# Performance work log

Measured on AMD Instinct MI355X. Metric: run time of the kernel, lower is better.

Reference implementation:

```python
import jax, jax.numpy as jnp
import numpy as np

B, Q, HID = 2, 2048, 2048
HQ, HKV, D = 16, 4, 128
EPS = 1e-6
THETA = 1000000.0


def _rmsnorm(x, w):
    # x: [..., D]
    return x * jax.lax.rsqrt(jnp.mean(x * x, axis=-1, keepdims=True) + EPS) * w


def _rope(x, cos, sin):
    # neox-style: split halves. x: [B,Q,H,D], cos/sin: [B,Q,1,D/2]
    d2 = x.shape[-1] // 2
    x1, x2 = x[..., :d2], x[..., d2:]
    return jnp.concatenate([x1 * cos - x2 * sin, x2 * cos + x1 * sin], axis=-1)


def setup_inputs() -> dict:
    key = jax.random.key(0)
    k1, k2, k3 = jax.random.split(key, 3)
    positions = jnp.broadcast_to(jnp.arange(Q, dtype=jnp.int32), (B, Q))
    hidden_states = jax.random.normal(k1, (B, Q, HID), dtype=jnp.float32)
    k_cache = jnp.zeros((B, HKV, Q, D), dtype=jnp.float32)
    v_cache = jnp.zeros((B, HKV, Q, D), dtype=jnp.float32)
    wqkv = jax.random.normal(k2, (HQ * D + 2 * HKV * D, HID), dtype=jnp.float32) * (HID ** -0.5)
    wo = jax.random.normal(k3, (HID, HQ * D), dtype=jnp.float32) * ((HQ * D) ** -0.5)
    q_norm_w = jnp.ones((D,), dtype=jnp.float32)
    k_norm_w = jnp.ones((D,), dtype=jnp.float32)
    return {"positions": positions, "hidden_states": hidden_states, "k_cache": k_cache,
            "v_cache": v_cache, "wqkv": wqkv, "wo": wo, "q_norm_w": q_norm_w,
            "k_norm_w": k_norm_w, "seq_len": Q}


def reference(positions, hidden_states, k_cache, v_cache, wqkv, wo, q_norm_w, k_norm_w, seq_len):
    bsz, qlen, _ = hidden_states.shape
    q_size, kv_size = HQ * D, HKV * D
    scale = D ** -0.5

    qkv = hidden_states.reshape(bsz * qlen, HID) @ wqkv.T  # [B*Q, q+2kv]
    q = qkv[:, :q_size].reshape(bsz, qlen, HQ, D)
    k = qkv[:, q_size:q_size + kv_size].reshape(bsz, qlen, HKV, D)
    v = qkv[:, q_size + kv_size:].reshape(bsz, qlen, HKV, D)

    q = _rmsnorm(q, q_norm_w)
    k = _rmsnorm(k, k_norm_w)

    inv_freq = 1.0 / (THETA ** (jnp.arange(0, D, 2, dtype=jnp.float32) / D))  # [D/2]
    freqs = positions.astype(jnp.float32)[..., None] * inv_freq  # [B,Q,D/2]
    cos = jnp.cos(freqs)[:, :, None, :]
    sin = jnp.sin(freqs)[:, :, None, :]
    q = _rope(q, cos, sin)
    k = _rope(k, cos, sin)

    q = q.transpose(0, 2, 1, 3)  # [B,HQ,Q,D]
    k = k.transpose(0, 2, 1, 3)  # [B,HKV,Q,D]
    v = v.transpose(0, 2, 1, 3)

    start = seq_len - qlen
    k_cache = jax.lax.dynamic_update_slice(k_cache, k, (0, 0, start, 0))
    v_cache = jax.lax.dynamic_update_slice(v_cache, v, (0, 0, start, 0))
    k_full = k_cache[:, :, :seq_len, :]
    v_full = v_cache[:, :, :seq_len, :]

    rep = HQ // HKV
    kf = jnp.repeat(k_full, rep, axis=1)  # [B,HQ,S,D]
    vf = jnp.repeat(v_full, rep, axis=1)

    scores = jnp.einsum('bhqd,bhkd->bhqk', q, kf) * scale
    if qlen == seq_len:  # is_causal path
        causal = jnp.tril(jnp.ones((qlen, seq_len), dtype=bool))
        scores = jnp.where(causal, scores, jnp.finfo(scores.dtype).min)
    attn = jax.nn.softmax(scores, axis=-1)
    out = jnp.einsum('bhqk,bhkd->bhqd', attn, vf)  # [B,HQ,Q,D]
    out = out.transpose(0, 2, 1, 3).reshape(bsz * qlen, HQ * D)
    return (out @ wo.T).reshape(bsz, qlen, HID)
```

## Files before the change

### kernel.cpp

```cpp
#include <hip/hip_runtime.h>

#define B_    2
#define Q_    2048
#define HID_  2048
#define HQ_   16
#define HKV_  4
#define D_    128
#define QSC_  (0.08838834764831843f * 1.4426950408889634f)
#define LOG2_THETA 19.931568569324174f
#define FMAX_ 20.0f

typedef unsigned short u16;
typedef __attribute__((ext_vector_type(8))) short bf16x8;
typedef __attribute__((ext_vector_type(4))) float f32x4;

__device__ __forceinline__ u16 f2bf(float x) {
  union { float f; unsigned int u; } v; v.f = x;
  unsigned int r = v.u + 0x7FFFu + ((v.u >> 16) & 1u);
  return (u16)(r >> 16);
}
__device__ __forceinline__ u16 f2bf_t(float x) {
  union { float f; unsigned int u; } v; v.f = x;
  return (u16)(v.u >> 16);
}

__device__ __forceinline__ void gl2lds16(u16* lds, const u16* g) {
  __builtin_amdgcn_global_load_lds((const __attribute__((address_space(1))) void*)g,
                                   (__attribute__((address_space(3))) void*)lds,
                                   16, 0, 0);
}

#define N4_HID  2097152
#define N4_WQKV 1572864
#define N4_WO   1048576
#define N4_ALL  (N4_HID + N4_WQKV + N4_WO)
#define NROPE   (B_ * Q_ * 64)
__global__ __launch_bounds__(256) void cvt_all(const float* __restrict__ h,
                                               const float* __restrict__ wq,
                                               const float* __restrict__ wo,
                                               const int* __restrict__ pos,
                                               u16* __restrict__ oh,
                                               u16* __restrict__ owq,
                                               u16* __restrict__ owo,
                                               float* __restrict__ rope) {
  int i = blockIdx.x * 256 + threadIdx.x;
  if (i >= N4_ALL) {
    int j = i - N4_ALL;
    int d = j & 63, row = j >> 6;
    float p = (float)pos[row];
    float inv = exp2f(-(float)d * (LOG2_THETA / 64.f));
    float sn, cn;
    sincosf(p * inv, &sn, &cn);
    ((float2*)rope)[j] = make_float2(cn, sn);
    return;
  }
  const float* src; u16* dst; int off;
  if (i < N4_HID)                 { src = h;  dst = oh;  off = i; }
  else if (i < N4_HID + N4_WQKV)  { src = wq; dst = owq; off = i - N4_HID; }
  else                            { src = wo; dst = owo; off = i - N4_HID - N4_WQKV; }
  float4 v = *(const float4*)(src + (size_t)off * 4);
  ushort4 o;
  o.x = f2bf(v.x); o.y = f2bf(v.y); o.z = f2bf(v.z); o.w = f2bf(v.w);
  *(ushort4*)(dst + (size_t)off * 4) = o;
}

__global__ __launch_bounds__(256) void gemm_qkv(const u16* __restrict__ A,
                                                const u16* __restrict__ Bw,
                                                const float* __restrict__ rope,
                                                const float* __restrict__ qw,
                                                const float* __restrict__ kw,
                                                u16* __restrict__ qb,
                                                u16* __restrict__ kb,
                                                u16* __restrict__ vt) {
  __shared__ __align__(16) u16 lds[12288];
  u16* As = lds;
  u16* Bs = lds + 4096;
  const int tid = threadIdx.x;
  const int wv = tid >> 6, lane = tid & 63;
  const int c = lane & 15, quad = lane >> 4;
  const int lr = lane >> 2, lp = lane & 3;
  const int lpg = (lp + 4 - ((lr >> 1) & 3)) & 3;
  const int swq = ((quad + (c >> 1)) & 3) * 8;
  const int m0 = blockIdx.x * 128;
  const int by = blockIdx.y;
  const int n0 = by * 128;
  f32x4 acc[2][8] = {};
  for (int k0 = 0; k0 < HID_; k0 += 32) {
    __syncthreads();
#pragma unroll
    for (int i = 0; i < 2; i++) {
      int r = wv * 16 + i * 64 + lr;
      gl2lds16(As + (size_t)(wv * 64 + i * 256) * 8,
               A + (size_t)(m0 + r) * HID_ + k0 + lpg * 8);
      gl2lds16(Bs + (size_t)(wv * 64 + i * 256) * 8,
               Bw + (size_t)(n0 + r) * HID_ + k0 + lpg * 8);
    }
    __syncthreads();
    bf16x8 af[2], bfr[8];
#pragma unroll
    for (int mi = 0; mi < 2; mi++)
      af[mi] = *(const bf16x8*)(As + (wv * 32 + mi * 16 + c) * 32 + swq);
#pragma unroll
    for (int ni = 0; ni < 8; ni++)
      bfr[ni] = *(const bf16x8*)(Bs + (ni * 16 + c) * 32 + swq);
#pragma unroll
    for (int mi = 0; mi < 2; mi++)
#pragma unroll
      for (int ni = 0; ni < 8; ni++)
        acc[mi][ni] = __builtin_amdgcn_mfma_f32_16x16x32_bf16(af[mi], bfr[ni],
                                                              acc[mi][ni], 0, 0, 0);
  }
  __syncthreads();

  if (by < 20) {
    const bool isq = by < 16;
    const float* w = isq ? qw : kw;
    const float osc = isq ? QSC_ : 1.f;
    float wl[8];
#pragma unroll
    for (int ni = 0; ni < 8; ni++) wl[ni] = w[ni * 16 + c];
    u16* dstbuf = isq ? qb : kb;
    const int hbase = isq ? by : (by - 16);
    const int nheads = isq ? HQ_ : HKV_;
#pragma unroll
    for (int ph = 0; ph < 2; ph++) {
      if (ph) __syncthreads();
      if ((wv >> 1) == ph) {
#pragma unroll
        for (int mi = 0; mi < 2; mi++)
#pragma unroll
          for (int r = 0; r < 4; r++) {
            const int row = m0 + wv * 32 + mi * 16 + quad * 4 + r;
            const int q = row & (Q_ - 1), b = row >> 11;
            float ss = 0.f;
#pragma unroll
            for (int ni = 0; ni < 8; ni++) ss += acc[mi][ni][r] * acc[mi][ni][r];
            ss += __shfl_xor(ss, 1); ss += __shfl_xor(ss, 2);
            ss += __shfl_xor(ss, 4); ss += __shfl_xor(ss, 8);
            const float rn = rsqrtf(ss * (1.f / 128.f) + 1e-6f) * osc;
            u16* lrow = lds + ((wv & 1) * 32 + mi * 16 + quad * 4 + r) * 132;
#pragma unroll
            for (int ni = 0; ni < 4; ni++) {
              float2 cssn = *(const float2*)(rope +
                  ((size_t)(b * Q_ + q) * 64 + ni * 16 + c) * 2);
              float x1 = acc[mi][ni][r]     * wl[ni]     * rn;
              float x2 = acc[mi][ni + 4][r] * wl[ni + 4] * rn;
              lrow[ni * 16 + c]       = f2bf(x1 * cssn.x - x2 * cssn.y);
              lrow[(ni + 4) * 16 + c] = f2bf(x2 * cssn.x + x1 * cssn.y);
            }
          }
      }
      __syncthreads();
      const int rowg = m0 + ph * 64 + (tid >> 2);
      const int q = rowg & (Q_ - 1), b = rowg >> 11;
      u16* dst = dstbuf + (((size_t)(b * nheads) + hbase) * Q_ + q) * D_ + (tid & 3) * 32;
      const u16* srcl = lds + (tid >> 2) * 132 + (tid & 3) * 32;
#pragma unroll
      for (int j = 0; j < 4; j++)
        *(bf16x8*)(dst + j * 8) = *(const bf16x8*)(srcl + j * 8);
    }
  } else {
    const int hk = by - 20;
    const int bb = m0 >> 11, q0 = m0 & (Q_ - 1);
    u16* vw = lds + wv * 3072;
#pragma unroll
    for (int mi = 0; mi < 2; mi++) {
      if (mi) __syncthreads();
#pragma unroll
      for (int ni = 0; ni < 8; ni++) {
        short4 pv;
        pv.x = (short)f2bf(acc[mi][ni][0]); pv.y = (short)f2bf(acc[mi][ni][1]);
        pv.z = (short)f2bf(acc[mi][ni][2]); pv.w = (short)f2bf(acc[mi][ni][3]);
        *(short4*)(vw + (ni * 16 + c) * 24 + quad * 4) = pv;
      }
      __syncthreads();
#pragma unroll
      for (int it = 0; it < 2; it++) {
        const int d = it * 64 + lane;
        const u16* src = vw + d * 24;
        u16* dst = vt + (((size_t)(bb * HKV_) + hk) * D_ + d) * Q_ +
                   q0 + wv * 32 + mi * 16;
        *(bf16x8*)(dst)     = *(const bf16x8*)(src);
        *(bf16x8*)(dst + 8) = *(const bf16x8*)(src + 8);
      }
    }
  }
}

__global__ __launch_bounds__(512) void gemm_bt8(const u16* __restrict__ A,
                                                const u16* __restrict__ Bw,
                                                float* __restrict__ C,
                                                int M, int N, int K) {
  __shared__ __align__(16) u16 lds[65536];
  const int tid = threadIdx.x;
  const int wv = tid >> 6, lane = tid & 63;
  const int wm = wv >> 2, wn = wv & 3;
  const int c = lane & 15, quad = lane >> 4;
  const int m0 = blockIdx.x * 256, n0 = blockIdx.y * 256;
  const int xg = ((lane & 7) ^ (lane >> 3)) * 8;
  const int x0 = ((quad)     ^ (c & 7)) * 8;
  const int x1 = ((quad | 4) ^ (c & 7)) * 8;
  const int aoff = wm * 8192 + c * 64;
  const int boff = 32768 + (wn >> 1) * 8192 + (wn & 1) * 4096 + c * 64;
  const u16* Ag = A  + (size_t)m0 * K;
  const u16* Bg = Bw + (size_t)n0 * K;
  const int NIT = K >> 7;

#define STG8(base, g, h, kt, buf)                                             \
  { _Pragma("unroll")                                                         \
    for (int j = 0; j < 2; ++j) {                                             \
      const int s = j * 8 + wv;                                               \
      gl2lds16(lds + (base) + (buf) * 16384 + (h) * 8192 + s * 512,           \
               (g) + (size_t)((h) * 128 + s * 8 + (lane >> 3)) * K            \
                   + (kt) * 64 + xg);                                         \
    } }
#define STG_A8(h, kt, buf) STG8(0,     Ag, h, kt, buf)
#define STG_B8(h, kt, buf) STG8(32768, Bg, h, kt, buf)
#define BAR8()  asm volatile("s_barrier" ::: "memory")
#define WLG8()  { asm volatile("s_waitcnt lgkmcnt(0)" ::: "memory");          \
                  __builtin_amdgcn_sched_barrier(0); }
#define WVM8(n) { asm volatile("s_waitcnt vmcnt(" #n ")" ::: "memory");       \
                  __builtin_amdgcn_sched_barrier(0); }
#define MFMA8(MF, NF, KS) acc[MF][NF] = __builtin_amdgcn_mfma_f32_16x16x32_bf16( \
                  fA[(MF) & 3][KS], fB[NF][KS], acc[MF][NF], 0, 0, 0)

  f32x4 acc[8][4] = {};
  bf16x8 fA[4][2], fB[4][2];

  STG_A8(0, 0, 0); STG_A8(1, 0, 0); STG_B8(0, 0, 0); STG_B8(1, 0, 0);
  STG_B8(0, 1, 1); STG_A8(0, 1, 1);
  WVM8(4);
  BAR8();

#pragma unroll 1
  for (int it = 0; it < NIT; ++it) {
    const bool last = (it == NIT - 1);
    const int kt1 = 2 * it + 1, kt2 = 2 * it + 2, kt3 = 2 * it + 3;

#pragma unroll
    for (int mf = 0; mf < 4; ++mf) {
      fA[mf][0] = *(const bf16x8*)(lds + aoff + mf * 1024 + x0);
      fA[mf][1] = *(const bf16x8*)(lds + aoff + mf * 1024 + x1);
    }
#pragma unroll
    for (int nf = 0; nf < 2; ++nf) {
      fB[nf][0] = *(const bf16x8*)(lds + boff + nf * 1024 + x0);
      fB[nf][1] = *(const bf16x8*)(lds + boff + nf * 1024 + x1);
    }
    STG_A8(1, kt1, 1);
    BAR8(); WLG8();
    __builtin_amdgcn_s_setprio(1);
#pragma unroll
    for (int mf = 0; mf < 4; ++mf)
#pragma unroll
      for (int nf = 0; nf < 2; ++nf) { MFMA8(mf, nf, 0); MFMA8(mf, nf, 1); }
    __builtin_amdgcn_s_setprio(0);
    BAR8();

#pragma unroll
    for (int nf = 2; nf < 4; ++nf) {
      fB[nf][0] = *(const bf16x8*)(lds + boff + nf * 1024 + x0);
      fB[nf][1] = *(const bf16x8*)(lds + boff + nf * 1024 + x1);
    }
    STG_B8(1, kt1, 1);
    BAR8(); WLG8();
    __builtin_amdgcn_s_setprio(1);
#pragma unroll
    for (int mf = 0; mf < 4; ++mf)
#pragma unroll
      for (int nf = 2; nf < 4; ++nf) { MFMA8(mf, nf, 0); MFMA8(mf, nf, 1); }
    __builtin_amdgcn_s_setprio(0);
    BAR8();

#pragma unroll
    for (int mf = 0; mf < 4; ++mf) {
      fA[mf][0] = *(const bf16x8*)(lds + aoff + (4 + mf) * 1024 + x0);
      fA[mf][1] = *(const bf16x8*)(lds + aoff + (4 + mf) * 1024 + x1);
    }
    if (!last) STG_B8(0, kt2, 0);
    BAR8(); WLG8();
    __builtin_amdgcn_s_setprio(1);
#pragma unroll
    for (int mf = 4; mf < 8; ++mf)
#pragma unroll
      for (int nf = 2; nf < 4; ++nf) { MFMA8(mf, nf, 0); MFMA8(mf, nf, 1); }
    __builtin_amdgcn_s_setprio(0);
    BAR8();

    if (!last) STG_A8(0, kt2, 0);
    BAR8(); WLG8();
    __builtin_amdgcn_s_setprio(1);
#pragma unroll
    for (int mf = 4; mf < 8; ++mf)
#pragma unroll
      for (int nf = 0; nf < 2; ++nf) { MFMA8(mf, nf, 0); MFMA8(mf, nf, 1); }
    __builtin_amdgcn_s_setprio(0);
    if (last) { WVM8(0); } else { WVM8(4); }
    BAR8();

#pragma unroll
    for (int mf = 0; mf < 4; ++mf) {
      fA[mf][0] = *(const bf16x8*)(lds + 16384 + aoff + mf * 1024 + x0);
      fA[mf][1] = *(const bf16x8*)(lds + 16384 + aoff + mf * 1024 + x1);
    }
#pragma unroll
    for (int nf = 0; nf < 2; ++nf) {
      fB[nf][0] = *(const bf16x8*)(lds + 16384 + boff + nf * 1024 + x0);
      fB[nf][1] = *(const bf16x8*)(lds + 16384 + boff + nf * 1024 + x1);
    }
    if (!last) STG_A8(1, kt2, 0);
    BAR8(); WLG8();
    __builtin_amdgcn_s_setprio(1);
#pragma unroll
    for (int mf = 0; mf < 4; ++mf)
#pragma unroll
      for (int nf = 0; nf < 2; ++nf) { MFMA8(mf, nf, 0); MFMA8(mf, nf, 1); }
    __builtin_amdgcn_s_setprio(0);
    BAR8();

#pragma unroll
    for (int nf = 2; nf < 4; ++nf) {
      fB[nf][0] = *(const bf16x8*)(lds + 16384 + boff + nf * 1024 + x0);
      fB[nf][1] = *(const bf16x8*)(lds + 16384 + boff + nf * 1024 + x1);
    }
    if (!last) STG_B8(1, kt2, 0);
    BAR8(); WLG8();
    __builtin_amdgcn_s_setprio(1);
#pragma unroll
    for (int mf = 0; mf < 4; ++mf)
#pragma unroll
      for (int nf = 2; nf < 4; ++nf) { MFMA8(mf, nf, 0); MFMA8(mf, nf, 1); }
    __builtin_amdgcn_s_setprio(0);
    BAR8();

#pragma unroll
    for (int mf = 0; mf < 4; ++mf) {
      fA[mf][0] = *(const bf16x8*)(lds + 16384 + aoff + (4 + mf) * 1024 + x0);
      fA[mf][1] = *(const bf16x8*)(lds + 16384 + aoff + (4 + mf) * 1024 + x1);
    }
    if (!last) STG_B8(0, kt3, 1);
    BAR8(); WLG8();
    __builtin_amdgcn_s_setprio(1);
#pragma unroll
    for (int mf = 4; mf < 8; ++mf)
#pragma unroll
      for (int nf = 2; nf < 4; ++nf) { MFMA8(mf, nf, 0); MFMA8(mf, nf, 1); }
    __builtin_amdgcn_s_setprio(0);
    BAR8();

    if (!last) STG_A8(0, kt3, 1);
    BAR8(); WLG8();
    __builtin_amdgcn_s_setprio(1);
#pragma unroll
    for (int mf = 4; mf < 8; ++mf)
#pragma unroll
      for (int nf = 0; nf < 2; ++nf) { MFMA8(mf, nf, 0); MFMA8(mf, nf, 1); }
    __builtin_amdgcn_s_setprio(0);
    if (last) { WVM8(0); } else { WVM8(4); }
    BAR8();
  }

  const int crow = m0 + wm * 128 + quad * 4;
  const int ccol = n0 + wn * 64 + c;
#pragma unroll
  for (int mf = 0; mf < 8; ++mf)
#pragma unroll
    for (int nf = 0; nf < 4; ++nf)
#pragma unroll
      for (int r = 0; r < 4; ++r)
        C[(size_t)(crow + mf * 16 + r) * N + ccol + nf * 16] = acc[mf][nf][r];
#undef STG8
#undef STG_A8
#undef STG_B8
#undef BAR8
#undef WLG8
#undef WVM8
#undef MFMA8
}

__global__ __launch_bounds__(256) void attn_fwd(const u16* __restrict__ qb,
                                                const u16* __restrict__ kb,
                                                const u16* __restrict__ vt,
                                                u16* __restrict__ ob) {
  __shared__ __align__(16) u16 lds[8192 + 8192 + 4608];
  u16* Ks = lds;
  u16* Vs = lds + 8192;
  u16* Ps = lds + 16384;
  const int p = blockIdx.x, h = blockIdx.y, b = blockIdx.z;
  const int hk = h >> 2;
  const int tid = threadIdx.x, wave = tid >> 6, lane = tid & 63;
  const int c = lane & 15, quad = lane >> 4;
  const int lr = lane >> 2, lp = lane & 3;
  const int lpg = (lp + 4 - ((lr >> 1) & 3)) & 3;
  const int swq = ((quad + (c >> 1)) & 3) * 8;
  const u16* qg = qb + ((size_t)b * HQ_ + h) * (size_t)Q_ * D_;
  const u16* kg = kb + ((size_t)b * HKV_ + hk) * (size_t)Q_ * D_;
  const u16* vg = vt + ((size_t)b * HKV_ + hk) * (size_t)D_ * Q_;
  u16* Pw = Ps + wave * 1152;
  u16* Bw = Ks + wave * 2176;

#pragma unroll 1
  for (int tp = 0; tp < 2; tp++) {
    const int t = tp ? (31 - p) : p;
    const int q0 = t * 64;
    const int qrow = q0 + wave * 16 + c;
    bf16x8 qf[4];
#pragma unroll
    for (int kk = 0; kk < 4; kk++)
      qf[kk] = *(const bf16x8*)(qg + (size_t)qrow * D_ + kk * 32 + quad * 8);
    f32x4 Oa[8] = {};
    float l_acc = 0.f;

#pragma unroll 1
    for (int kt = 0; kt <= t; kt++) {
      __syncthreads();
#pragma unroll
      for (int i = 0; i < 4; i++) {
        gl2lds16(Ks + (size_t)(i * 256 + wave * 64) * 8,
                 kg + ((size_t)kt * 64 + wave * 16 + lr) * D_ + i * 32 + lpg * 8);
        int d = (i & 1) * 64 + wave * 16 + lr;
        gl2lds16(Vs + (size_t)(i * 256 + wave * 64) * 8,
                 vg + (size_t)d * Q_ + kt * 64 + (i >> 1) * 32 + lpg * 8);
      }
      __syncthreads();
      f32x4 S[4];
#pragma unroll
      for (int n = 0; n < 4; n++) {
        f32x4 a = {-FMAX_, -FMAX_, -FMAX_, -FMAX_};
#pragma unroll
        for (int kk = 0; kk < 4; kk++) {
          bf16x8 kf = *(const bf16x8*)(Ks + kk * 2048 + (n * 16 + c) * 32 + swq);
          a = __builtin_amdgcn_mfma_f32_16x16x32_bf16(kf, qf[kk], a, 0, 0, 0);
        }
        S[n] = a;
      }
      if (kt == t) {
#pragma unroll
        for (int n = 0; n < 4; n++)
#pragma unroll
          for (int r = 0; r < 4; r++) {
            int key = kt * 64 + n * 16 + quad * 4 + r;
            if (key > qrow) S[n][r] = -1e9f;
          }
      }
#pragma unroll
      for (int n = 0; n < 4; n++) {
        float p0 = __builtin_amdgcn_exp2f(S[n][0]);
        float p1 = __builtin_amdgcn_exp2f(S[n][1]);
        float p2 = __builtin_amdgcn_exp2f(S[n][2]);
        float p3 = __builtin_amdgcn_exp2f(S[n][3]);
        l_acc += (p0 + p1) + (p2 + p3);
        short4 pk;
        pk.x = (short)f2bf_t(p0); pk.y = (short)f2bf_t(p1);
        pk.z = (short)f2bf_t(p2); pk.w = (short)f2bf_t(p3);
        *(short4*)(Pw + c * 72 + n * 16 + quad * 4) = pk;
      }
      bf16x8 pf[2];
#pragma unroll
      for (int kk2 = 0; kk2 < 2; kk2++)
        pf[kk2] = *(const bf16x8*)(Pw + c * 72 + kk2 * 32 + quad * 8);
#pragma unroll
      for (int md = 0; md < 8; md++)
#pragma unroll
        for (int kk2 = 0; kk2 < 2; kk2++) {
          bf16x8 vf = *(const bf16x8*)(Vs + kk2 * 4096 + (md * 16 + c) * 32 + swq);
          Oa[md] = __builtin_amdgcn_mfma_f32_16x16x32_bf16(vf, pf[kk2], Oa[md], 0, 0, 0);
        }
    }
    float l_row = l_acc;
    l_row += __shfl_xor(l_row, 16);
    l_row += __shfl_xor(l_row, 32);
    __syncthreads();
    const float invl = 1.f / l_row;
#pragma unroll
    for (int md = 0; md < 8; md++) {
      short4 ok;
      ok.x = (short)f2bf(Oa[md][0] * invl); ok.y = (short)f2bf(Oa[md][1] * invl);
      ok.z = (short)f2bf(Oa[md][2] * invl); ok.w = (short)f2bf(Oa[md][3] * invl);
      *(short4*)(Bw + c * 136 + md * 16 + quad * 4) = ok;
    }
    const int orow = q0 + wave * 16 + lr;
#pragma unroll
    for (int tt = 0; tt < 4; tt++) {
      bf16x8 ov = *(const bf16x8*)(Bw + lr * 136 + lp * 32 + tt * 8);
      *(bf16x8*)(ob + ((size_t)(b * Q_ + orow) * HQ_ + h) * D_ + lp * 32 + tt * 8) = ov;
    }
  }
}

extern "C" void kernel_launch(void* const* d_in, const int* in_sizes, int n_in,
                              void* d_out, int out_size, void* d_ws, size_t ws_size,
                              hipStream_t stream) {
  const int*   positions = (const int*)  d_in[0];
  const float* hidden    = (const float*)d_in[1];
  const float* wqkv      = (const float*)d_in[4];
  const float* wo        = (const float*)d_in[5];
  const float* qnw       = (const float*)d_in[6];
  const float* knw       = (const float*)d_in[7];
  char* ws = (char*)d_ws;
  u16*   hid_bf  = (u16*)(ws);
  u16*   wqkv_bf = (u16*)(ws + 16777216);
  u16*   wo_bf   = (u16*)(ws + 29360128);
  u16*   q_bf    = (u16*)(ws + 37748736);
  u16*   k_bf    = (u16*)(ws + 54525952);
  u16*   vt_bf   = (u16*)(ws + 58720256);
  float* rope    = (float*)(ws + 62914560);
  u16*   attn_bf = hid_bf;

  cvt_all<<<19456, 256, 0, stream>>>(hidden, wqkv, wo, positions,
                                     hid_bf, wqkv_bf, wo_bf, rope);
  gemm_qkv<<<dim3(32, 24), 256, 0, stream>>>(hid_bf, wqkv_bf, rope, qnw, knw,
                                             q_bf, k_bf, vt_bf);
  attn_fwd<<<dim3(16, 16, 2), 256, 0, stream>>>(q_bf, k_bf, vt_bf, attn_bf);
  gemm_bt8<<<dim3(16, 8), 512, 0, stream>>>(attn_bf, wo_bf, (float*)d_out,
                                            4096, 2048, 2048);
}
```

Baseline: 336.8 us.

## Rewrite QKV GEMM as 256x256 8-wave double-buffered pipelined kernel

Replaces the 128x128 single-stage QKV projection GEMM with a 256x256-tile, 512-thread kernel modelled on the existing output-projection GEMM. It uses double-buffered LDS with staggered global-to-LDS loads, swizzled fragments, explicit waitcnt/barrier scheduling and raised MFMA priority. The RMSNorm+RoPE and V-transpose epilogues are reworked to per-wave LDS staging. The aim is to raise operand reuse and overlap memory with compute, at the cost of a grid of only 192 blocks, which may underfill the GPU's compute units.

```diff
diff --git a/kernel.cpp b/kernel.cpp
--- a/kernel.cpp
+++ b/kernel.cpp
@@ -64,127 +64,271 @@
   *(ushort4*)(dst + (size_t)off * 4) = o;
 }
 
-__global__ __launch_bounds__(256) void gemm_qkv(const u16* __restrict__ A,
-                                                const u16* __restrict__ Bw,
-                                                const float* __restrict__ rope,
-                                                const float* __restrict__ qw,
-                                                const float* __restrict__ kw,
-                                                u16* __restrict__ qb,
-                                                u16* __restrict__ kb,
-                                                u16* __restrict__ vt) {
-  __shared__ __align__(16) u16 lds[12288];
-  u16* As = lds;
-  u16* Bs = lds + 4096;
+__global__ __launch_bounds__(512) void gemm_qkv8(const u16* __restrict__ A,
+                                                 const u16* __restrict__ Bw,
+                                                 const float* __restrict__ rope,
+                                                 const float* __restrict__ qw,
+                                                 const float* __restrict__ kw,
+                                                 u16* __restrict__ qb,
+                                                 u16* __restrict__ kb,
+                                                 u16* __restrict__ vt) {
+  __shared__ __align__(16) u16 lds[65536];
   const int tid = threadIdx.x;
   const int wv = tid >> 6, lane = tid & 63;
+  const int wm = wv >> 1, wn = wv & 1;
   const int c = lane & 15, quad = lane >> 4;
-  const int lr = lane >> 2, lp = lane & 3;
-  const int lpg = (lp + 4 - ((lr >> 1) & 3)) & 3;
-  const int swq = ((quad + (c >> 1)) & 3) * 8;
-  const int m0 = blockIdx.x * 128;
+  const int m0 = blockIdx.x * 256;
   const int by = blockIdx.y;
-  const int n0 = by * 128;
-  f32x4 acc[2][8] = {};
-  for (int k0 = 0; k0 < HID_; k0 += 32) {
-    __syncthreads();
-#pragma unroll
-    for (int i = 0; i < 2; i++) {
-      int r = wv * 16 + i * 64 + lr;
-      gl2lds16(As + (size_t)(wv * 64 + i * 256) * 8,
-               A + (size_t)(m0 + r) * HID_ + k0 + lpg * 8);
-      gl2lds16(Bs + (size_t)(wv * 64 + i * 256) * 8,
-               Bw + (size_t)(n0 + r) * HID_ + k0 + lpg * 8);
-    }
-    __syncthreads();
-    bf16x8 af[2], bfr[8];
-#pragma unroll
-    for (int mi = 0; mi < 2; mi++)
-      af[mi] = *(const bf16x8*)(As + (wv * 32 + mi * 16 + c) * 32 + swq);
-#pragma unroll
-    for (int ni = 0; ni < 8; ni++)
-      bfr[ni] = *(const bf16x8*)(Bs + (ni * 16 + c) * 32 + swq);
-#pragma unroll
-    for (int mi = 0; mi < 2; mi++)
-#pragma unroll
-      for (int ni = 0; ni < 8; ni++)
-        acc[mi][ni] = __builtin_amdgcn_mfma_f32_16x16x32_bf16(af[mi], bfr[ni],
-                                                              acc[mi][ni], 0, 0, 0);
+  const int n0 = by * 256;
+  const int xg = ((lane & 7) ^ (lane >> 3)) * 8;
+  const int x0 = ((quad)     ^ (c & 7)) * 8;
+  const int x1 = ((quad | 4) ^ (c & 7)) * 8;
+  const int aoff = (wm >> 1) * 8192 + (wm & 1) * 4096 + c * 64;
+  const int boff = 32768 + wn * 8192 + c * 64;
+  const u16* Ag = A  + (size_t)m0 * HID_;
+  const u16* Bg = Bw + (size_t)n0 * HID_;
+  const int NIT = HID_ >> 7;
+
+#define STGQ(base, g, h, kt, buf)                                             \
+  { _Pragma("unroll")                                                         \
+    for (int j = 0; j < 2; ++j) {                                             \
+      const int s = j * 8 + wv;                                               \
+      gl2lds16(lds + (base) + (buf) * 16384 + (h) * 8192 + s * 512,           \
+               (g) + (size_t)((h) * 128 + s * 8 + (lane >> 3)) * HID_         \
+                   + (kt) * 64 + xg);                                         \
+    } }
+#define STGQ_A(h, kt, buf) STGQ(0,     Ag, h, kt, buf)
+#define STGQ_B(h, kt, buf) STGQ(32768, Bg, h, kt, buf)
+#define BARQ()  asm volatile("s_barrier" ::: "memory")
+#define WLGQ()  { asm volatile("s_waitcnt lgkmcnt(0)" ::: "memory");          \
+                  __builtin_amdgcn_sched_barrier(0); }
+#define WVMQ(n) { asm volatile("s_waitcnt vmcnt(" #n ")" ::: "memory");       \
+                  __builtin_amdgcn_sched_barrier(0); }
+#define MMQ(MF, NF, FA, MI) {                                                 \
+  acc[MF][NF] = __builtin_amdgcn_mfma_f32_16x16x32_bf16(FA[MI][0], fB[(NF)&3][0], \
+                                                        acc[MF][NF], 0, 0, 0);\
+  acc[MF][NF] = __builtin_amdgcn_mfma_f32_16x16x32_bf16(FA[MI][1], fB[(NF)&3][1], \
+                                                        acc[MF][NF], 0, 0, 0); }
+
+  f32x4 acc[4][8] = {};
+  bf16x8 fAa[2][2], fAb[2][2], fB[4][2];
+
+  STGQ_A(0, 0, 0); STGQ_A(1, 0, 0); STGQ_B(0, 0, 0); STGQ_B(1, 0, 0);
+  STGQ_A(0, 1, 1); STGQ_B(0, 1, 1);
+  WVMQ(4);
+  BARQ();
+
+#pragma unroll 1
+  for (int it = 0; it < NIT; ++it) {
+    const bool last = (it == NIT - 1);
+    const int kt1 = 2 * it + 1, kt2 = 2 * it + 2, kt3 = 2 * it + 3;
+
+#pragma unroll
+    for (int mi = 0; mi < 2; ++mi) {
+      fAa[mi][0] = *(const bf16x8*)(lds + aoff + mi * 1024 + x0);
+      fAa[mi][1] = *(const bf16x8*)(lds + aoff + mi * 1024 + x1);
+    }
+#pragma unroll
+    for (int nf = 0; nf < 4; ++nf) {
+      fB[nf][0] = *(const bf16x8*)(lds + boff + nf * 1024 + x0);
+      fB[nf][1] = *(const bf16x8*)(lds + boff + nf * 1024 + x1);
+    }
+    STGQ_A(1, kt1, 1);
+    BARQ(); WLGQ();
+    __builtin_amdgcn_s_setprio(1);
+#pragma unroll
+    for (int mi = 0; mi < 2; ++mi)
+#pragma unroll
+      for (int nf = 0; nf < 4; ++nf) MMQ(mi, nf, fAa, mi);
+    __builtin_amdgcn_s_setprio(0);
+    BARQ();
+
+#pragma unroll
+    for (int mi = 0; mi < 2; ++mi) {
+      fAb[mi][0] = *(const bf16x8*)(lds + aoff + (2 + mi) * 1024 + x0);
+      fAb[mi][1] = *(const bf16x8*)(lds + aoff + (2 + mi) * 1024 + x1);
+    }
+    STGQ_B(1, kt1, 1);
+    BARQ(); WLGQ();
+    __builtin_amdgcn_s_setprio(1);
+#pragma unroll
+    for (int mi = 0; mi < 2; ++mi)
+#pragma unroll
+      for (int nf = 0; nf < 4; ++nf) MMQ(2 + mi, nf, fAb, mi);
+    __builtin_amdgcn_s_setprio(0);
+    BARQ();
+
+#pragma unroll
+    for (int nf = 0; nf < 4; ++nf) {
+      fB[nf][0] = *(const bf16x8*)(lds + boff + (4 + nf) * 1024 + x0);
+      fB[nf][1] = *(const bf16x8*)(lds + boff + (4 + nf) * 1024 + x1);
+    }
+    if (!last) STGQ_A(0, kt2, 0);
+    BARQ(); WLGQ();
+    __builtin_amdgcn_s_setprio(1);
+#pragma unroll
+    for (int mi = 0; mi < 2; ++mi)
+#pragma unroll
+      for (int nf = 4; nf < 8; ++nf) MMQ(2 + mi, nf, fAb, mi);
+    __builtin_amdgcn_s_setprio(0);
+    BARQ();
+
+    if (!last) STGQ_B(0, kt2, 0);
+    BARQ(); WLGQ();
+    __builtin_amdgcn_s_setprio(1);
+#pragma unroll
+    for (int mi = 0; mi < 2; ++mi)
+#pragma unroll
+      for (int nf = 4; nf < 8; ++nf) MMQ(mi, nf, fAa, mi);
+    __builtin_amdgcn_s_setprio(0);
+    if (last) { WVMQ(0); } else { WVMQ(4); }
+    BARQ();
+
+#pragma unroll
+    for (int mi = 0; mi < 2; ++mi) {
+      fAa[mi][0] = *(const bf16x8*)(lds + 16384 + aoff + mi * 1024 + x0);
+      fAa[mi][1] = *(const bf16x8*)(lds + 16384 + aoff + mi * 1024 + x1);
+    }
+#pragma unroll
+    for (int nf = 0; nf < 4; ++nf) {
+      fB[nf][0] = *(const bf16x8*)(lds + 16384 + boff + nf * 1024 + x0);
+      fB[nf][1] = *(const bf16x8*)(lds + 16384 + boff + nf * 1024 + x1);
+    }
+    if (!last) STGQ_A(1, kt2, 0);
+    BARQ(); WLGQ();
+    __builtin_amdgcn_s_setprio(1);
+#pragma unroll
+    for (int mi = 0; mi < 2; ++mi)
+#pragma unroll
+      for (int nf = 0; nf < 4; ++nf) MMQ(mi, nf, fAa, mi);
+    __builtin_amdgcn_s_setprio(0);
+    BARQ();
+
+#pragma unroll
+    for (int mi = 0; mi < 2; ++mi) {
+      fAb[mi][0] = *(const bf16x8*)(lds + 16384 + aoff + (2 + mi) * 1024 + x0);
+      fAb[mi][1] = *(const bf16x8*)(lds + 16384 + aoff + (2 + mi) * 1024 + x1);
+    }
+    if (!last) STGQ_B(1, kt2, 0);
+    BARQ(); WLGQ();
+    __builtin_amdgcn_s_setprio(1);
+#pragma unroll
+    for (int mi = 0; mi < 2; ++mi)
+#pragma unroll
+      for (int nf = 0; nf < 4; ++nf) MMQ(2 + mi, nf, fAb, mi);
+    __builtin_amdgcn_s_setprio(0);
+    BARQ();
+
+#pragma unroll
+    for (int nf = 0; nf < 4; ++nf) {
+      fB[nf][0] = *(const bf16x8*)(lds + 16384 + boff + (4 + nf) * 1024 + x0);
+      fB[nf][1] = *(const bf16x8*)(lds + 16384 + boff + (4 + nf) * 1024 + x1);
+    }
+    if (!last) STGQ_A(0, kt3, 1);
+    BARQ(); WLGQ();
+    __builtin_amdgcn_s_setprio(1);
+#pragma unroll
+    for (int mi = 0; mi < 2; ++mi)
+#pragma unroll
+      for (int nf = 4; nf < 8; ++nf) MMQ(2 + mi, nf, fAb, mi);
+    __builtin_amdgcn_s_setprio(0);
+    BARQ();
+
+    if (!last) STGQ_B(0, kt3, 1);
+    BARQ(); WLGQ();
+    __builtin_amdgcn_s_setprio(1);
+#pragma unroll
+    for (int mi = 0; mi < 2; ++mi)
+#pragma unroll
+      for (int nf = 4; nf < 8; ++nf) MMQ(mi, nf, fAa, mi);
+    __builtin_amdgcn_s_setprio(0);
+    if (last) { WVMQ(0); } else { WVMQ(4); }
+    BARQ();
   }
-  __syncthreads();
-
-  if (by < 20) {
-    const bool isq = by < 16;
+
+  const int h = by * 2 + wn;
+  if (h < 20) {
+    const bool isq = h < 16;
     const float* w = isq ? qw : kw;
     const float osc = isq ? QSC_ : 1.f;
     float wl[8];
 #pragma unroll
-    for (int ni = 0; ni < 8; ni++) wl[ni] = w[ni * 16 + c];
+    for (int nf = 0; nf < 8; ++nf) wl[nf] = w[nf * 16 + c];
     u16* dstbuf = isq ? qb : kb;
-    const int hbase = isq ? by : (by - 16);
+    const int hbase = isq ? h : (h - 16);
     const int nheads = isq ? HQ_ : HKV_;
-#pragma unroll
-    for (int ph = 0; ph < 2; ph++) {
-      if (ph) __syncthreads();
-      if ((wv >> 1) == ph) {
-#pragma unroll
-        for (int mi = 0; mi < 2; mi++)
-#pragma unroll
-          for (int r = 0; r < 4; r++) {
-            const int row = m0 + wv * 32 + mi * 16 + quad * 4 + r;
-            const int q = row & (Q_ - 1), b = row >> 11;
-            float ss = 0.f;
-#pragma unroll
-            for (int ni = 0; ni < 8; ni++) ss += acc[mi][ni][r] * acc[mi][ni][r];
-            ss += __shfl_xor(ss, 1); ss += __shfl_xor(ss, 2);
-            ss += __shfl_xor(ss, 4); ss += __shfl_xor(ss, 8);
-            const float rn = rsqrtf(ss * (1.f / 128.f) + 1e-6f) * osc;
-            u16* lrow = lds + ((wv & 1) * 32 + mi * 16 + quad * 4 + r) * 132;
-#pragma unroll
-            for (int ni = 0; ni < 4; ni++) {
-              float2 cssn = *(const float2*)(rope +
-                  ((size_t)(b * Q_ + q) * 64 + ni * 16 + c) * 2);
-              float x1 = acc[mi][ni][r]     * wl[ni]     * rn;
-              float x2 = acc[mi][ni + 4][r] * wl[ni + 4] * rn;
-              lrow[ni * 16 + c]       = f2bf(x1 * cssn.x - x2 * cssn.y);
-              lrow[(ni + 4) * 16 + c] = f2bf(x2 * cssn.x + x1 * cssn.y);
-            }
+    u16* lw = lds + wv * 4224;
+#pragma unroll
+    for (int pass = 0; pass < 2; ++pass) {
+#pragma unroll
+      for (int mi = 0; mi < 2; ++mi) {
+        const int mf = pass * 2 + mi;
+#pragma unroll
+        for (int r = 0; r < 4; ++r) {
+          const int row = m0 + wm * 64 + mf * 16 + quad * 4 + r;
+          const int q = row & (Q_ - 1), b = row >> 11;
+          float ss = 0.f;
+#pragma unroll
+          for (int nf = 0; nf < 8; ++nf) ss += acc[mf][nf][r] * acc[mf][nf][r];
+          ss += __shfl_xor(ss, 1); ss += __shfl_xor(ss, 2);
+          ss += __shfl_xor(ss, 4); ss += __shfl_xor(ss, 8);
+          const float rn = rsqrtf(ss * (1.f / 128.f) + 1e-6f) * osc;
+          u16* lrow = lw + (mi * 16 + quad * 4 + r) * 132;
+#pragma unroll
+          for (int ni = 0; ni < 4; ni++) {
+            float2 cssn = *(const float2*)(rope +
+                ((size_t)(b * Q_ + q) * 64 + ni * 16 + c) * 2);
+            float x1 = acc[mf][ni][r]     * wl[ni]     * rn;
+            float x2 = acc[mf][ni + 4][r] * wl[ni + 4] * rn;
+            lrow[ni * 16 + c]       = f2bf(x1 * cssn.x - x2 * cssn.y);
+            lrow[(ni + 4) * 16 + c] = f2bf(x2 * cssn.x + x1 * cssn.y);
           }
-      }
-      __syncthreads();
-      const int rowg = m0 + ph * 64 + (tid >> 2);
-      const int q = rowg & (Q_ - 1), b = rowg >> 11;
-      u16* dst = dstbuf + (((size_t)(b * nheads) + hbase) * Q_ + q) * D_ + (tid & 3) * 32;
-      const u16* srcl = lds + (tid >> 2) * 132 + (tid & 3) * 32;
-#pragma unroll
-      for (int j = 0; j < 4; j++)
-        *(bf16x8*)(dst + j * 8) = *(const bf16x8*)(srcl + j * 8);
+        }
+      }
+#pragma unroll
+      for (int itr = 0; itr < 8; ++itr) {
+        const int rl = itr * 4 + quad;
+        const int rowg = m0 + wm * 64 + pass * 32 + rl;
+        const int q = rowg & (Q_ - 1), b = rowg >> 11;
+        u16* dst = dstbuf + (((size_t)(b * nheads) + hbase) * Q_ + q) * D_ + c * 8;
+        *(bf16x8*)dst = *(const bf16x8*)(lw + rl * 132 + c * 8);
+      }
     }
   } else {
-    const int hk = by - 20;
-    const int bb = m0 >> 11, q0 = m0 & (Q_ - 1);
-    u16* vw = lds + wv * 3072;
-#pragma unroll
-    for (int mi = 0; mi < 2; mi++) {
-      if (mi) __syncthreads();
-#pragma unroll
-      for (int ni = 0; ni < 8; ni++) {
-        short4 pv;
-        pv.x = (short)f2bf(acc[mi][ni][0]); pv.y = (short)f2bf(acc[mi][ni][1]);
-        pv.z = (short)f2bf(acc[mi][ni][2]); pv.w = (short)f2bf(acc[mi][ni][3]);
-        *(short4*)(vw + (ni * 16 + c) * 24 + quad * 4) = pv;
-      }
-      __syncthreads();
-#pragma unroll
-      for (int it = 0; it < 2; it++) {
-        const int d = it * 64 + lane;
-        const u16* src = vw + d * 24;
+    const int hk = h - 20;
+    const int bb = m0 >> 11;
+    const int q0w = (m0 & (Q_ - 1)) + wm * 64;
+    u16* lw = lds + wv * 4352;
+#pragma unroll
+    for (int pass = 0; pass < 2; ++pass) {
+#pragma unroll
+      for (int nfl = 0; nfl < 4; ++nfl) {
+        const int nf = pass * 4 + nfl;
+#pragma unroll
+        for (int mf = 0; mf < 4; ++mf) {
+          short4 pv;
+          pv.x = (short)f2bf(acc[mf][nf][0]); pv.y = (short)f2bf(acc[mf][nf][1]);
+          pv.z = (short)f2bf(acc[mf][nf][2]); pv.w = (short)f2bf(acc[mf][nf][3]);
+          *(short4*)(lw + (nfl * 16 + c) * 68 + mf * 16 + quad * 4) = pv;
+        }
+      }
+#pragma unroll
+      for (int itr = 0; itr < 8; ++itr) {
+        const int dl = itr * 8 + (lane >> 3);
+        const int d = pass * 64 + dl;
         u16* dst = vt + (((size_t)(bb * HKV_) + hk) * D_ + d) * Q_ +
-                   q0 + wv * 32 + mi * 16;
-        *(bf16x8*)(dst)     = *(const bf16x8*)(src);
-        *(bf16x8*)(dst + 8) = *(const bf16x8*)(src + 8);
+                   q0w + (lane & 7) * 8;
+        *(bf16x8*)dst = *(const bf16x8*)(lw + dl * 68 + (lane & 7) * 8);
       }
     }
   }
+#undef STGQ
+#undef STGQ_A
+#undef STGQ_B
+#undef BARQ
+#undef WLGQ
+#undef WVMQ
+#undef MMQ
 }
 
 __global__ __launch_bounds__(512) void gemm_bt8(const u16* __restrict__ A,
@@ -509,8 +653,8 @@
 
   cvt_all<<<19456, 256, 0, stream>>>(hidden, wqkv, wo, positions,
                                      hid_bf, wqkv_bf, wo_bf, rope);
-  gemm_qkv<<<dim3(32, 24), 256, 0, stream>>>(hid_bf, wqkv_bf, rope, qnw, knw,
-                                             q_bf, k_bf, vt_bf);
+  gemm_qkv8<<<dim3(16, 12), 512, 0, stream>>>(hid_bf, wqkv_bf, rope, qnw, knw,
+                                              q_bf, k_bf, vt_bf);
   attn_fwd<<<dim3(16, 16, 2), 256, 0, stream>>>(q_bf, k_bf, vt_bf, attn_bf);
   gemm_bt8<<<dim3(16, 8), 512, 0, stream>>>(attn_bf, wo_bf, (float*)d_out,
                                             4096, 2048, 2048);
```

After: 309.1 us. 8.2% less time.
